# Optimization experiments

Measured on AMD Instinct MI355X. Metric: run time of the kernel, lower is better.

Reference implementation:

```python
import jax, jax.numpy as jnp
import numpy as np

B, C, CI, HM, HC = 4, 64, 32, 128, 64  # batch, in_channels, inter_channels, main HW, cross HW
BN_EPS = 1e-5


def conv1x1(x, w, b):
    # x: [B,Cin,H,W], w: [Cout,Cin], b: [Cout]
    return jnp.einsum('bchw,oc->bohw', x, w) + b[None, :, None, None]


def _lin_coords(n_in, n_out):
    # PyTorch bilinear, align_corners=False: src = (i+0.5)*scale - 0.5, clamped
    scale = n_in / n_out
    src = (jnp.arange(n_out, dtype=jnp.float32) + 0.5) * scale - 0.5
    src = jnp.clip(src, 0.0, n_in - 1)
    i0 = jnp.floor(src).astype(jnp.int32)
    i1 = jnp.minimum(i0 + 1, n_in - 1)
    w = src - i0.astype(jnp.float32)
    return i0, i1, w


def resize_bilinear(x, h_out, w_out):
    # x: [B,C,H,W] -> [B,C,h_out,w_out], matches torch F.interpolate(mode='bilinear', align_corners=False)
    _, _, h_in, w_in = x.shape
    i0, i1, wh = _lin_coords(h_in, h_out)
    x = x[:, :, i0, :] * (1.0 - wh)[None, None, :, None] + x[:, :, i1, :] * wh[None, None, :, None]
    j0, j1, ww = _lin_coords(w_in, w_out)
    x = x[:, :, :, j0] * (1.0 - ww)[None, None, None, :] + x[:, :, :, j1] * ww[None, None, None, :]
    return x


def setup_inputs() -> dict:
    key = jax.random.key(0)
    ks = jax.random.split(key, 12)
    p = lambda k, shape, s=0.05: jax.random.normal(k, shape, dtype=jnp.float32) * s
    return {
        'main_feature': jax.random.normal(ks[0], (B, C, HM, HM), dtype=jnp.float32),
        'cross_feature': jax.random.normal(ks[1], (B, C, HC, HC), dtype=jnp.float32),
        'g_w': p(ks[2], (CI, C)), 'g_b': p(ks[3], (CI,)),
        'theta_w': p(ks[4], (CI, C)), 'theta_b': p(ks[5], (CI,)),
        'phi_w': p(ks[6], (CI, C)), 'phi_b': p(ks[7], (CI,)),
        'w_w': p(ks[8], (C, CI)), 'w_b': p(ks[9], (C,)),
        'bn_gamma': 1.0 + p(ks[10], (C,)), 'bn_beta': p(ks[11], (C,)),
    }


def reference(main_feature, cross_feature, g_w, g_b, theta_w, theta_b,
              phi_w, phi_b, w_w, w_b, bn_gamma, bn_beta):
    b, _, hc, wc = cross_feature.shape
    hm = main_feature.shape[2]
    # g(cross) -> [B, Nc, Ci]
    x = conv1x1(cross_feature, g_w, g_b).reshape(b, CI, -1).transpose(0, 2, 1)
    # theta(cross) -> [B, Ci, Nc]
    y = conv1x1(cross_feature, theta_w, theta_b).reshape(b, CI, -1)
    # phi(resize(main -> cross size)) -> [B, Nc, Ci]
    z = resize_bilinear(main_feature, hc, hc)
    z = conv1x1(z, phi_w, phi_b).reshape(b, CI, -1).transpose(0, 2, 1)
    # unscaled attention: [B, Nc, Nc]
    f = jnp.einsum('bnc,bcm->bnm', x, y)
    attn = jax.nn.softmax(f, axis=-1)
    out = jnp.einsum('bnm,bmc->bnc', attn, z)           # [B, Nc, Ci]
    out = out.transpose(0, 2, 1).reshape(b, CI, hc, wc)  # [B, Ci, Hc, Wc]
    # W: 1x1 conv + BatchNorm2d (training mode: batch statistics, biased var)
    out = conv1x1(out, w_w, w_b)
    mean = out.mean(axis=(0, 2, 3), keepdims=True)
    var = out.var(axis=(0, 2, 3), keepdims=True)
    out = (out - mean) * jax.lax.rsqrt(var + BN_EPS)
    out = out * bn_gamma[None, :, None, None] + bn_beta[None, :, None, None]
    out = resize_bilinear(out, hm, hm)
    return out + main_feature
```

## Files before the change

### kernel.cpp

```cpp
#include <hip/hip_runtime.h>
#include <hip/hip_bf16.h>


typedef __attribute__((ext_vector_type(8))) short bf16x8;
typedef __attribute__((ext_vector_type(4))) float f32x4;
typedef __attribute__((ext_vector_type(16))) float f32x16;

#define LOG2E 1.4426950408889634f

static __device__ __forceinline__ unsigned short f2bf_bits(float x) {
    __hip_bfloat16 h = __float2bfloat16(x);
    return *(unsigned short*)&h;
}
static __device__ __forceinline__ unsigned int pk2bf(float a, float b) {
    __hip_bfloat162 h = __float22bfloat162_rn(make_float2(a, b));
    return *(unsigned int*)&h;
}

__global__ __launch_bounds__(256) void qkv_kernel(
    const float* __restrict__ cross, const float* __restrict__ mainf,
    const float* __restrict__ g_w,  const float* __restrict__ g_b,
    const float* __restrict__ th_w, const float* __restrict__ th_b,
    const float* __restrict__ ph_w, const float* __restrict__ ph_b,
    __hip_bfloat16* __restrict__ Qb, __hip_bfloat16* __restrict__ Kb,
    __hip_bfloat16* __restrict__ Vt)
{
    __shared__ float xs[64][128];
    const int kind = blockIdx.x >> 7;
    const int sub  = blockIdx.x & 127;
    const int b    = sub >> 5;
    const int n0   = (sub & 31) << 7;
    const int tid  = threadIdx.x;
    const float* w  = (kind == 0) ? g_w : (kind == 1) ? th_w : ph_w;
    const float* bs = (kind == 0) ? g_b : (kind == 1) ? th_b : ph_b;

    if (kind < 2) {
        const float* src = cross + (((size_t)(b * 64)) << 12) + n0;
        const int jr = (tid & 31) << 2, c0 = tid >> 5;
#pragma unroll
        for (int it = 0; it < 8; ++it) {
            int c = (it << 3) | c0;
            *(float4*)&xs[c][jr] = *(const float4*)(src + ((size_t)c << 12) + jr);
        }
    } else {
        const int px = tid & 127, chh = tid >> 7;
        const int n = n0 + px;
        const int i2 = (n >> 6) << 1, j2 = (n & 63) << 1;
        const float* src = mainf + (((size_t)(b * 64)) << 14) + i2 * 128 + j2;
#pragma unroll 4
        for (int cc = 0; cc < 32; ++cc) {
            int c = (chh << 5) | cc;
            const float2 a = *(const float2*)(src + ((size_t)c << 14));
            const float2 d = *(const float2*)(src + ((size_t)c << 14) + 128);
            xs[c][px] = 0.25f * ((a.x + a.y) + (d.x + d.y));
        }
    }
    __syncthreads();

    const int px = tid & 127, cih = tid >> 7, ci0 = cih << 4;
    float acc[16];
#pragma unroll
    for (int j = 0; j < 16; ++j) acc[j] = bs[ci0 + j];
#pragma unroll 4
    for (int c = 0; c < 64; ++c) {
        float x = xs[c][px];
#pragma unroll
        for (int j = 0; j < 16; ++j)
            acc[j] = fmaf(w[((ci0 + j) << 6) + c], x, acc[j]);
    }
    const int n = n0 + px;
    const int pix = (b << 12) + n;
    if (kind < 2) {
        if (kind == 0) {
#pragma unroll
            for (int j = 0; j < 16; ++j) acc[j] *= LOG2E;
        }
        unsigned int u[8];
#pragma unroll
        for (int i = 0; i < 8; ++i)
            u[i] = (unsigned int)f2bf_bits(acc[2 * i]) |
                   ((unsigned int)f2bf_bits(acc[2 * i + 1]) << 16);
        uint4* d4 = (uint4*)(((kind == 0) ? Qb : Kb) + (size_t)pix * 32 + ci0);
        d4[0] = make_uint4(u[0], u[1], u[2], u[3]);
        d4[1] = make_uint4(u[4], u[5], u[6], u[7]);
    } else {
#pragma unroll
        for (int j = 0; j < 16; ++j)
            Vt[((size_t)((b << 5) | (ci0 + j)) << 12) + n] = __float2bfloat16(acc[j]);
    }
}

__global__ __launch_bounds__(256) void attn_mfma(
    const __hip_bfloat16* __restrict__ Qb, const __hip_bfloat16* __restrict__ Kb,
    const __hip_bfloat16* __restrict__ Vt, const float* __restrict__ w_w,
    const float* __restrict__ w_b, float* __restrict__ out2)
{
    __shared__ __align__(16) float redbuf[3][64][20];
    __shared__ __align__(16) float obuf[32][36];
    const int tid = threadIdx.x, lane = tid & 63, w = tid >> 6;
    const int q = lane & 31, h = lane >> 5;
    const int b = blockIdx.y, qbase = blockIdx.x << 5;
    const int sig = (q & ~12) | ((q & 4) << 1) | ((q & 8) >> 1);

    const __hip_bfloat16* Qrow = Qb + (((size_t)(b << 12) + qbase + q) << 5);
    const bf16x8 bq1 = *(const bf16x8*)(Qrow + 8 * h);
    const bf16x8 bq2 = *(const bf16x8*)(Qrow + 16 + 8 * h);

    const __hip_bfloat16* Kbb = Kb + ((size_t)(b << 12) << 5);
    const __hip_bfloat16* Vbb = Vt + ((size_t)(b << 5) << 12) + ((size_t)q << 12);
    const int kq = w << 10;
#define LDK1(k) (*(const bf16x8*)(Kbb + ((size_t)((k) + sig) << 5) + 8 * h))
#define LDK2(k) (*(const bf16x8*)(Kbb + ((size_t)((k) + sig) << 5) + 16 + 8 * h))
#define LDV1(k) (*(const bf16x8*)(Vbb + (k) + 8 * h))
#define LDV2(k) (*(const bf16x8*)(Vbb + (k) + 16 + 8 * h))

    f32x16 acc;
#pragma unroll
    for (int r = 0; r < 16; ++r) acc[r] = 0.f;
    const f32x16 z16 = acc;
    float den = 0.f;

    bf16x8 a1c = LDK1(kq),      a2c = LDK2(kq);
    bf16x8 v1B = LDV1(kq),      v2B = LDV2(kq);
    bf16x8 a1n = LDK1(kq + 32), a2n = LDK2(kq + 32);
    bf16x8 v1N = LDV1(kq + 32), v2N = LDV2(kq + 32);
    bf16x8 ap1, ap2, v1A, v2A;

    {
        f32x16 s = __builtin_amdgcn_mfma_f32_32x32x16_bf16(a1c, bq1, z16, 0, 0, 0);
        s = __builtin_amdgcn_mfma_f32_32x32x16_bf16(a2c, bq2, s, 0, 0, 0);
        float e[16];
#pragma unroll
        for (int r = 0; r < 16; ++r) e[r] = __builtin_amdgcn_exp2f(s[r]);
        den += (((e[0]+e[1])+(e[2]+e[3])) + ((e[4]+e[5])+(e[6]+e[7])))
             + (((e[8]+e[9])+(e[10]+e[11])) + ((e[12]+e[13])+(e[14]+e[15])));
        uint4 t1 = make_uint4(pk2bf(e[0],e[1]), pk2bf(e[2],e[3]),
                              pk2bf(e[4],e[5]), pk2bf(e[6],e[7]));
        uint4 t2 = make_uint4(pk2bf(e[8],e[9]), pk2bf(e[10],e[11]),
                              pk2bf(e[12],e[13]), pk2bf(e[14],e[15]));
        ap1 = *(bf16x8*)&t1; ap2 = *(bf16x8*)&t2;
    }

#pragma unroll 2
    for (int ch = 1; ch < 32; ++ch) {
        const int kn = kq + ((ch + 1) & 31) * 32;
        v1A = v1B; v2A = v2B;
        v1B = v1N; v2B = v2N;
        a1c = a1n; a2c = a2n;
        a1n = LDK1(kn); a2n = LDK2(kn);
        v1N = LDV1(kn); v2N = LDV2(kn);

        f32x16 s = __builtin_amdgcn_mfma_f32_32x32x16_bf16(a1c, bq1, z16, 0, 0, 0);
        s = __builtin_amdgcn_mfma_f32_32x32x16_bf16(a2c, bq2, s, 0, 0, 0);

        acc = __builtin_amdgcn_mfma_f32_32x32x16_bf16(ap1, v1A, acc, 0, 0, 0);
        acc = __builtin_amdgcn_mfma_f32_32x32x16_bf16(ap2, v2A, acc, 0, 0, 0);

        float e[16];
#pragma unroll
        for (int r = 0; r < 16; ++r) e[r] = __builtin_amdgcn_exp2f(s[r]);
        den += (((e[0]+e[1])+(e[2]+e[3])) + ((e[4]+e[5])+(e[6]+e[7])))
             + (((e[8]+e[9])+(e[10]+e[11])) + ((e[12]+e[13])+(e[14]+e[15])));
        uint4 t1 = make_uint4(pk2bf(e[0],e[1]), pk2bf(e[2],e[3]),
                              pk2bf(e[4],e[5]), pk2bf(e[6],e[7]));
        uint4 t2 = make_uint4(pk2bf(e[8],e[9]), pk2bf(e[10],e[11]),
                              pk2bf(e[12],e[13]), pk2bf(e[14],e[15]));
        ap1 = *(bf16x8*)&t1; ap2 = *(bf16x8*)&t2;
    }
    acc = __builtin_amdgcn_mfma_f32_32x32x16_bf16(ap1, v1B, acc, 0, 0, 0);
    acc = __builtin_amdgcn_mfma_f32_32x32x16_bf16(ap2, v2B, acc, 0, 0, 0);
#undef LDK1
#undef LDK2
#undef LDV1
#undef LDV2

    den += __shfl_xor(den, 32);

    if (w) {
        float* rb = &redbuf[w - 1][lane][0];
        f32x4* rb4 = (f32x4*)rb;
#pragma unroll
        for (int p = 0; p < 4; ++p) {
            f32x4 t = {acc[4*p], acc[4*p+1], acc[4*p+2], acc[4*p+3]};
            rb4[p] = t;
        }
        rb[16] = den;
    }
    __syncthreads();
    if (w == 0) {
#pragma unroll
        for (int ww = 0; ww < 3; ++ww) {
            const float* rb = &redbuf[ww][lane][0];
            const f32x4* rb4 = (const f32x4*)rb;
#pragma unroll
            for (int p = 0; p < 4; ++p) {
                f32x4 t = rb4[p];
                acc[4*p] += t[0]; acc[4*p+1] += t[1];
                acc[4*p+2] += t[2]; acc[4*p+3] += t[3];
            }
            den += rb[16];
        }
#pragma unroll
        for (int r = 0; r < 16; ++r) {
            int qr = (r & 3) + 8 * (r >> 2) + 4 * h;
            float inv = 1.0f / __shfl(den, qr);
            obuf[qr][q] = acc[r] * inv;
        }
    }
    __syncthreads();

    const int qq = tid & 31, cog = tid >> 5;
    float ov[32];
    const float4* orow = (const float4*)&obuf[qq][0];
#pragma unroll
    for (int k4 = 0; k4 < 8; ++k4) {
        float4 t = orow[k4];
        ov[4*k4] = t.x; ov[4*k4+1] = t.y; ov[4*k4+2] = t.z; ov[4*k4+3] = t.w;
    }
    float* dstbase = out2 + (((size_t)(b << 6)) << 12) + qbase + qq;
#pragma unroll
    for (int kk = 0; kk < 8; ++kk) {
        int co = (kk << 3) | cog;
        const float4* wr = (const float4*)&w_w[co << 5];
        float acc2 = w_b[co];
#pragma unroll
        for (int k4 = 0; k4 < 8; ++k4) {
            float4 t = wr[k4];
            acc2 = fmaf(t.x, ov[4*k4],   acc2);
            acc2 = fmaf(t.y, ov[4*k4+1], acc2);
            acc2 = fmaf(t.z, ov[4*k4+2], acc2);
            acc2 = fmaf(t.w, ov[4*k4+3], acc2);
        }
        dstbase[(size_t)co << 12] = acc2;
    }
}

__global__ __launch_bounds__(256) void stats_kernel(
    const float* __restrict__ out2, float* __restrict__ stats1)
{
    int co = blockIdx.x >> 2, b = blockIdx.x & 3, t = threadIdx.x;
    const float* p = out2 + ((size_t)((b << 6) | co) << 12);
    float s = 0.f, s2 = 0.f;
#pragma unroll
    for (int ii = 0; ii < 16; ++ii) {
        float v = p[(ii << 8) | t];
        s += v; s2 = fmaf(v, v, s2);
    }
    __shared__ float rs[256], rs2[256];
    rs[t] = s; rs2[t] = s2;
    __syncthreads();
    for (int off = 128; off > 0; off >>= 1) {
        if (t < off) { rs[t] += rs[t + off]; rs2[t] += rs2[t + off]; }
        __syncthreads();
    }
    if (t == 0) {
        stats1[blockIdx.x * 2]     = rs[0];
        stats1[blockIdx.x * 2 + 1] = rs2[0];
    }
}

__global__ __launch_bounds__(256) void up_kernel(
    const float* __restrict__ out2, const float* __restrict__ stats1,
    const float* __restrict__ gamma, const float* __restrict__ beta,
    const float* __restrict__ mainf, float* __restrict__ out)
{
    int gid = blockIdx.x * 256 + threadIdx.x;
    int j4 = (gid & 31) << 2;
    int i  = (gid >> 5) & 127;
    int co = (gid >> 12) & 63;
    int b  = gid >> 18;

    float sm = 0.f, sq = 0.f;
#pragma unroll
    for (int bb = 0; bb < 4; ++bb) {
        sm += stats1[((co << 2) | bb) * 2];
        sq += stats1[((co << 2) | bb) * 2 + 1];
    }
    float mean = sm * (1.0f / 16384.0f);
    float var  = sq * (1.0f / 16384.0f) - mean * mean;
    float inv  = rsqrtf(var + 1e-5f);
    float scale = gamma[co] * inv;
    float shift = beta[co] - mean * scale;

    int ih = i >> 1;
    int k0, k1; float wi;
    if (i & 1)       { k0 = ih;     k1 = (ih < 63) ? ih + 1 : 63; wi = 0.25f; }
    else if (ih == 0){ k0 = 0;      k1 = 0;                       wi = 0.0f;  }
    else             { k0 = ih - 1; k1 = ih;                      wi = 0.75f; }

    const float* p0r = out2 + ((size_t)((b << 6) | co) << 12) + (k0 << 6);
    const float* p1r = out2 + ((size_t)((b << 6) | co) << 12) + (k1 << 6);

    float res[4];
#pragma unroll
    for (int jj = 0; jj < 4; ++jj) {
        int j = j4 | jj;
        int il = j >> 1;
        int l0, l1; float wj;
        if (j & 1)       { l0 = il;     l1 = (il < 63) ? il + 1 : 63; wj = 0.25f; }
        else if (il == 0){ l0 = 0;      l1 = 0;                       wj = 0.0f;  }
        else             { l0 = il - 1; l1 = il;                      wj = 0.75f; }
        float v00 = p0r[l0], v01 = p0r[l1];
        float v10 = p1r[l0], v11 = p1r[l1];
        float top = v00 + wj * (v01 - v00);
        float bot = v10 + wj * (v11 - v10);
        float v = top + wi * (bot - top);
        res[jj] = fmaf(v, scale, shift);
    }
    size_t idx = (((size_t)((b << 6) | co)) << 14) + (i << 7) + j4;
    float4 m4 = *(const float4*)(mainf + idx);
    *(float4*)(out + idx) = make_float4(res[0] + m4.x, res[1] + m4.y,
                                        res[2] + m4.z, res[3] + m4.w);
}

extern "C" void kernel_launch(void* const* d_in, const int* in_sizes, int n_in,
                              void* d_out, int out_size, void* d_ws, size_t ws_size,
                              hipStream_t stream)
{
    const float* mainf = (const float*)d_in[0];
    const float* cross = (const float*)d_in[1];
    const float* g_w   = (const float*)d_in[2];
    const float* g_b   = (const float*)d_in[3];
    const float* th_w  = (const float*)d_in[4];
    const float* th_b  = (const float*)d_in[5];
    const float* ph_w  = (const float*)d_in[6];
    const float* ph_b  = (const float*)d_in[7];
    const float* w_w   = (const float*)d_in[8];
    const float* w_b   = (const float*)d_in[9];
    const float* gamma = (const float*)d_in[10];
    const float* beta  = (const float*)d_in[11];
    float* out = (float*)d_out;

    __hip_bfloat16* Qb = (__hip_bfloat16*)d_ws;
    __hip_bfloat16* Kb = Qb + 524288;
    __hip_bfloat16* Vt = Kb + 524288;
    float* out2   = (float*)(Vt + 524288);
    float* stats1 = out2 + 1048576;

    qkv_kernel<<<384, 256, 0, stream>>>(cross, mainf, g_w, g_b, th_w, th_b,
                                        ph_w, ph_b, Qb, Kb, Vt);
    attn_mfma<<<dim3(128, 4), 256, 0, stream>>>(Qb, Kb, Vt, w_w, w_b, out2);
    stats_kernel<<<256, 256, 0, stream>>>(out2, stats1);
    up_kernel<<<4096, 256, 0, stream>>>(out2, stats1, gamma, beta, mainf, out);
}
```

Measured before the change: 148.6 us.

## Fuse BN statistics into attention epilogue and widen attention blocks to 8 waves

```diff
diff --git a/kernel.cpp b/kernel.cpp
--- a/kernel.cpp
+++ b/kernel.cpp
@@ -23,7 +23,7 @@
     const float* __restrict__ th_w, const float* __restrict__ th_b,
     const float* __restrict__ ph_w, const float* __restrict__ ph_b,
     __hip_bfloat16* __restrict__ Qb, __hip_bfloat16* __restrict__ Kb,
-    __hip_bfloat16* __restrict__ Vt)
+    __hip_bfloat16* __restrict__ Vt, float* __restrict__ stats1)
 {
     __shared__ float xs[64][128];
     const int kind = blockIdx.x >> 7;
@@ -33,6 +33,8 @@
     const int tid  = threadIdx.x;
     const float* w  = (kind == 0) ? g_w : (kind == 1) ? th_w : ph_w;
     const float* bs = (kind == 0) ? g_b : (kind == 1) ? th_b : ph_b;
+
+    if (blockIdx.x == 0 && tid < 128) stats1[tid] = 0.f;
 
     if (kind < 2) {
         const float* src = cross + (((size_t)(b * 64)) << 12) + n0;
@@ -90,12 +92,13 @@
     }
 }
 
-__global__ __launch_bounds__(256) void attn_mfma(
+__global__ __launch_bounds__(512, 4) void attn_mfma(
     const __hip_bfloat16* __restrict__ Qb, const __hip_bfloat16* __restrict__ Kb,
     const __hip_bfloat16* __restrict__ Vt, const float* __restrict__ w_w,
-    const float* __restrict__ w_b, float* __restrict__ out2)
+    const float* __restrict__ w_b, float* __restrict__ out2,
+    float* __restrict__ stats1)
 {
-    __shared__ __align__(16) float redbuf[3][64][20];
+    __shared__ __align__(16) float redbuf[7][64][20];
     __shared__ __align__(16) float obuf[32][36];
     const int tid = threadIdx.x, lane = tid & 63, w = tid >> 6;
     const int q = lane & 31, h = lane >> 5;
@@ -106,13 +109,15 @@
     const bf16x8 bq1 = *(const bf16x8*)(Qrow + 8 * h);
     const bf16x8 bq2 = *(const bf16x8*)(Qrow + 16 + 8 * h);
 
-    const __hip_bfloat16* Kbb = Kb + ((size_t)(b << 12) << 5);
-    const __hip_bfloat16* Vbb = Vt + ((size_t)(b << 5) << 12) + ((size_t)q << 12);
-    const int kq = w << 10;
-#define LDK1(k) (*(const bf16x8*)(Kbb + ((size_t)((k) + sig) << 5) + 8 * h))
-#define LDK2(k) (*(const bf16x8*)(Kbb + ((size_t)((k) + sig) << 5) + 16 + 8 * h))
-#define LDV1(k) (*(const bf16x8*)(Vbb + (k) + 8 * h))
-#define LDV2(k) (*(const bf16x8*)(Vbb + (k) + 16 + 8 * h))
+    const char* Kbase = (const char*)(Kb + ((size_t)(b << 12) << 5));
+    const char* Vbase = (const char*)(Vt + ((size_t)(b << 5) << 12));
+    const unsigned int offK0 = (unsigned int)((((w << 9) + sig) << 6) | (h << 4));
+    const unsigned int offV0 = (unsigned int)((q << 13) + (w << 10) + (h << 4));
+    unsigned int offK = offK0, offV = offV0;
+#define LDK1 (*(const bf16x8*)(Kbase + offK))
+#define LDK2 (*(const bf16x8*)(Kbase + offK + 32))
+#define LDV1 (*(const bf16x8*)(Vbase + offV))
+#define LDV2 (*(const bf16x8*)(Vbase + offV + 32))
 
     f32x16 acc;
 #pragma unroll
@@ -120,12 +125,11 @@
     const f32x16 z16 = acc;
     float den = 0.f;
 
-    bf16x8 a1c = LDK1(kq),      a2c = LDK2(kq);
-    bf16x8 v1B = LDV1(kq),      v2B = LDV2(kq);
-    bf16x8 a1n = LDK1(kq + 32), a2n = LDK2(kq + 32);
-    bf16x8 v1N = LDV1(kq + 32), v2N = LDV2(kq + 32);
-    bf16x8 ap1, ap2, v1A, v2A;
-
+    bf16x8 a1c = LDK1, a2c = LDK2, v1c = LDV1, v2c = LDV2;
+    offK += 2048; offV += 64;
+    bf16x8 a1n = LDK1, a2n = LDK2, v1n = LDV1, v2n = LDV2;
+
+    bf16x8 ap1, ap2;
     {
         f32x16 s = __builtin_amdgcn_mfma_f32_32x32x16_bf16(a1c, bq1, z16, 0, 0, 0);
         s = __builtin_amdgcn_mfma_f32_32x32x16_bf16(a2c, bq2, s, 0, 0, 0);
@@ -141,20 +145,18 @@
         ap1 = *(bf16x8*)&t1; ap2 = *(bf16x8*)&t2;
     }
 
-#pragma unroll 2
-    for (int ch = 1; ch < 32; ++ch) {
-        const int kn = kq + ((ch + 1) & 31) * 32;
-        v1A = v1B; v2A = v2B;
-        v1B = v1N; v2B = v2N;
-        a1c = a1n; a2c = a2n;
-        a1n = LDK1(kn); a2n = LDK2(kn);
-        v1N = LDV1(kn); v2N = LDV2(kn);
+#pragma unroll 3
+    for (int ch = 1; ch < 16; ++ch) {
+        acc = __builtin_amdgcn_mfma_f32_32x32x16_bf16(ap1, v1c, acc, 0, 0, 0);
+        acc = __builtin_amdgcn_mfma_f32_32x32x16_bf16(ap2, v2c, acc, 0, 0, 0);
+
+        a1c = a1n; a2c = a2n; v1c = v1n; v2c = v2n;
+        offK = (ch == 15) ? offK0 : offK + 2048;
+        offV = (ch == 15) ? offV0 : offV + 64;
+        a1n = LDK1; a2n = LDK2; v1n = LDV1; v2n = LDV2;
 
         f32x16 s = __builtin_amdgcn_mfma_f32_32x32x16_bf16(a1c, bq1, z16, 0, 0, 0);
         s = __builtin_amdgcn_mfma_f32_32x32x16_bf16(a2c, bq2, s, 0, 0, 0);
-
-        acc = __builtin_amdgcn_mfma_f32_32x32x16_bf16(ap1, v1A, acc, 0, 0, 0);
-        acc = __builtin_amdgcn_mfma_f32_32x32x16_bf16(ap2, v2A, acc, 0, 0, 0);
 
         float e[16];
 #pragma unroll
@@ -167,8 +169,8 @@
                               pk2bf(e[12],e[13]), pk2bf(e[14],e[15]));
         ap1 = *(bf16x8*)&t1; ap2 = *(bf16x8*)&t2;
     }
-    acc = __builtin_amdgcn_mfma_f32_32x32x16_bf16(ap1, v1B, acc, 0, 0, 0);
-    acc = __builtin_amdgcn_mfma_f32_32x32x16_bf16(ap2, v2B, acc, 0, 0, 0);
+    acc = __builtin_amdgcn_mfma_f32_32x32x16_bf16(ap1, v1c, acc, 0, 0, 0);
+    acc = __builtin_amdgcn_mfma_f32_32x32x16_bf16(ap2, v2c, acc, 0, 0, 0);
 #undef LDK1
 #undef LDK2
 #undef LDV1
@@ -189,7 +191,7 @@
     __syncthreads();
     if (w == 0) {
 #pragma unroll
-        for (int ww = 0; ww < 3; ++ww) {
+        for (int ww = 0; ww < 7; ++ww) {
             const float* rb = &redbuf[ww][lane][0];
             const f32x4* rb4 = (const f32x4*)rb;
 #pragma unroll
@@ -219,8 +221,8 @@
     }
     float* dstbase = out2 + (((size_t)(b << 6)) << 12) + qbase + qq;
 #pragma unroll
-    for (int kk = 0; kk < 8; ++kk) {
-        int co = (kk << 3) | cog;
+    for (int kk = 0; kk < 4; ++kk) {
+        int co = (kk << 4) | cog;
         const float4* wr = (const float4*)&w_w[co << 5];
         float acc2 = w_b[co];
 #pragma unroll
@@ -232,30 +234,16 @@
             acc2 = fmaf(t.w, ov[4*k4+3], acc2);
         }
         dstbase[(size_t)co << 12] = acc2;
-    }
-}
-
-__global__ __launch_bounds__(256) void stats_kernel(
-    const float* __restrict__ out2, float* __restrict__ stats1)
-{
-    int co = blockIdx.x >> 2, b = blockIdx.x & 3, t = threadIdx.x;
-    const float* p = out2 + ((size_t)((b << 6) | co) << 12);
-    float s = 0.f, s2 = 0.f;
-#pragma unroll
-    for (int ii = 0; ii < 16; ++ii) {
-        float v = p[(ii << 8) | t];
-        s += v; s2 = fmaf(v, v, s2);
-    }
-    __shared__ float rs[256], rs2[256];
-    rs[t] = s; rs2[t] = s2;
-    __syncthreads();
-    for (int off = 128; off > 0; off >>= 1) {
-        if (t < off) { rs[t] += rs[t + off]; rs2[t] += rs2[t + off]; }
-        __syncthreads();
-    }
-    if (t == 0) {
-        stats1[blockIdx.x * 2]     = rs[0];
-        stats1[blockIdx.x * 2 + 1] = rs2[0];
+        float s1 = acc2, s2 = acc2 * acc2;
+#pragma unroll
+        for (int m = 1; m < 32; m <<= 1) {
+            s1 += __shfl_xor(s1, m);
+            s2 += __shfl_xor(s2, m);
+        }
+        if (qq == 0) {
+            atomicAdd(&stats1[co << 1], s1);
+            atomicAdd(&stats1[(co << 1) | 1], s2);
+        }
     }
 }
 
@@ -270,12 +258,8 @@
     int co = (gid >> 12) & 63;
     int b  = gid >> 18;
 
-    float sm = 0.f, sq = 0.f;
-#pragma unroll
-    for (int bb = 0; bb < 4; ++bb) {
-        sm += stats1[((co << 2) | bb) * 2];
-        sq += stats1[((co << 2) | bb) * 2 + 1];
-    }
+    float sm = stats1[co << 1];
+    float sq = stats1[(co << 1) | 1];
     float mean = sm * (1.0f / 16384.0f);
     float var  = sq * (1.0f / 16384.0f) - mean * mean;
     float inv  = rsqrtf(var + 1e-5f);
@@ -338,8 +322,7 @@
     float* stats1 = out2 + 1048576;
 
     qkv_kernel<<<384, 256, 0, stream>>>(cross, mainf, g_w, g_b, th_w, th_b,
-                                        ph_w, ph_b, Qb, Kb, Vt);
-    attn_mfma<<<dim3(128, 4), 256, 0, stream>>>(Qb, Kb, Vt, w_w, w_b, out2);
-    stats_kernel<<<256, 256, 0, stream>>>(out2, stats1);
+                                        ph_w, ph_b, Qb, Kb, Vt, stats1);
+    attn_mfma<<<dim3(128, 4), 512, 0, stream>>>(Qb, Kb, Vt, w_w, w_b, out2, stats1);
     up_kernel<<<4096, 256, 0, stream>>>(out2, stats1, gamma, beta, mainf, out);
 }
```

Measured after the change: 268.3 us. 1.81x slower.

## Split attention key range across two blocks and combine partials in a separate kernel

Applied to the files above, without the earlier changes.

```diff
diff --git a/kernel.cpp b/kernel.cpp
--- a/kernel.cpp
+++ b/kernel.cpp
@@ -90,16 +90,15 @@
     }
 }
 
-__global__ __launch_bounds__(256) void attn_mfma(
+__global__ __launch_bounds__(256) void attn_part(
     const __hip_bfloat16* __restrict__ Qb, const __hip_bfloat16* __restrict__ Kb,
-    const __hip_bfloat16* __restrict__ Vt, const float* __restrict__ w_w,
-    const float* __restrict__ w_b, float* __restrict__ out2)
+    const __hip_bfloat16* __restrict__ Vt,
+    float* __restrict__ pnum, float* __restrict__ pden)
 {
     __shared__ __align__(16) float redbuf[3][64][20];
-    __shared__ __align__(16) float obuf[32][36];
     const int tid = threadIdx.x, lane = tid & 63, w = tid >> 6;
     const int q = lane & 31, h = lane >> 5;
-    const int b = blockIdx.y, qbase = blockIdx.x << 5;
+    const int b = blockIdx.y, qbase = blockIdx.x << 5, half = blockIdx.z;
     const int sig = (q & ~12) | ((q & 4) << 1) | ((q & 8) >> 1);
 
     const __hip_bfloat16* Qrow = Qb + (((size_t)(b << 12) + qbase + q) << 5);
@@ -108,7 +107,7 @@
 
     const __hip_bfloat16* Kbb = Kb + ((size_t)(b << 12) << 5);
     const __hip_bfloat16* Vbb = Vt + ((size_t)(b << 5) << 12) + ((size_t)q << 12);
-    const int kq = w << 10;
+    const int kq = (half << 11) + (w << 9);
 #define LDK1(k) (*(const bf16x8*)(Kbb + ((size_t)((k) + sig) << 5) + 8 * h))
 #define LDK2(k) (*(const bf16x8*)(Kbb + ((size_t)((k) + sig) << 5) + 16 + 8 * h))
 #define LDV1(k) (*(const bf16x8*)(Vbb + (k) + 8 * h))
@@ -142,8 +141,8 @@
     }
 
 #pragma unroll 2
-    for (int ch = 1; ch < 32; ++ch) {
-        const int kn = kq + ((ch + 1) & 31) * 32;
+    for (int ch = 1; ch < 16; ++ch) {
+        const int kn = kq + ((ch + 1) & 15) * 32;
         v1A = v1B; v2A = v2B;
         v1B = v1N; v2B = v2N;
         a1c = a1n; a2c = a2n;
@@ -200,12 +199,37 @@
             }
             den += rb[16];
         }
+        const int tile = (((half << 2) | b) << 7) | blockIdx.x;
+        float* pn = pnum + ((size_t)tile << 10);
 #pragma unroll
         for (int r = 0; r < 16; ++r) {
             int qr = (r & 3) + 8 * (r >> 2) + 4 * h;
-            float inv = 1.0f / __shfl(den, qr);
-            obuf[qr][q] = acc[r] * inv;
-        }
+            pn[(qr << 5) + q] = acc[r];
+        }
+        if (h == 0) pden[(tile << 5) + q] = den;
+    }
+}
+
+__global__ __launch_bounds__(256) void attn_combine(
+    const float* __restrict__ pnum, const float* __restrict__ pden,
+    const float* __restrict__ w_w, const float* __restrict__ w_b,
+    float* __restrict__ out2)
+{
+    __shared__ __align__(16) float obuf[32][36];
+    const int tid = threadIdx.x;
+    const int b = blockIdx.y, qbase = blockIdx.x << 5;
+    const int tile0 = ((b) << 7) | blockIdx.x;
+    const int tile1 = ((4 + b) << 7) | blockIdx.x;
+
+    const float* pn0 = pnum + ((size_t)tile0 << 10);
+    const float* pn1 = pnum + ((size_t)tile1 << 10);
+#pragma unroll
+    for (int k = 0; k < 4; ++k) {
+        int e = tid + (k << 8);
+        int qr = e >> 5, ci = e & 31;
+        float num = pn0[e] + pn1[e];
+        float den = pden[(tile0 << 5) + qr] + pden[(tile1 << 5) + qr];
+        obuf[qr][ci] = num * (1.0f / den);
     }
     __syncthreads();
 
@@ -336,10 +360,13 @@
     __hip_bfloat16* Vt = Kb + 524288;
     float* out2   = (float*)(Vt + 524288);
     float* stats1 = out2 + 1048576;
+    float* pnum   = stats1 + 512;
+    float* pden   = pnum + 1048576;
 
     qkv_kernel<<<384, 256, 0, stream>>>(cross, mainf, g_w, g_b, th_w, th_b,
                                         ph_w, ph_b, Qb, Kb, Vt);
-    attn_mfma<<<dim3(128, 4), 256, 0, stream>>>(Qb, Kb, Vt, w_w, w_b, out2);
+    attn_part<<<dim3(128, 4, 2), 256, 0, stream>>>(Qb, Kb, Vt, pnum, pden);
+    attn_combine<<<dim3(128, 4), 256, 0, stream>>>(pnum, pden, w_w, w_b, out2);
     stats_kernel<<<256, 256, 0, stream>>>(out2, stats1);
     up_kernel<<<4096, 256, 0, stream>>>(out2, stats1, gamma, beta, mainf, out);
 }
```

Measured after the change: 151.8 us. 2.2% more time.
